# Performance work log

Measured on AMD Instinct MI355X. Metric: run time of the kernel, lower is better.

Reference implementation:

```python
import jax, jax.numpy as jnp
import numpy as np

N_EMBD = 1024
NUM_HEADS = 16
HEAD_SIZE = 64
B, T, T_ENC = 2, 2048, 2048


def setup_inputs() -> dict:
    key = jax.random.key(0)
    k1, k2, k3, k4, k5 = jax.random.split(key, 5)
    scale = 1.0 / np.sqrt(N_EMBD)
    return {
        "x_enc": jax.random.normal(k1, (B, T_ENC, N_EMBD), dtype=jnp.float32),
        "x": jax.random.normal(k2, (B, T, N_EMBD), dtype=jnp.float32),
        "Wk": jax.random.normal(k3, (N_EMBD, NUM_HEADS * HEAD_SIZE), dtype=jnp.float32) * scale,
        "Wq": jax.random.normal(k4, (N_EMBD, NUM_HEADS * HEAD_SIZE), dtype=jnp.float32) * scale,
        "Wv": jax.random.normal(k5, (N_EMBD, NUM_HEADS * HEAD_SIZE), dtype=jnp.float32) * scale,
    }


def reference(x_enc, x, Wk, Wq, Wv):
    b, t, c = x.shape
    _, t_enc, _ = x_enc.shape
    # projections (bias-free linears)
    k = (x_enc @ Wk).reshape(b, t_enc, NUM_HEADS, HEAD_SIZE)  # [B,S,H,D]
    v = (x_enc @ Wv).reshape(b, t_enc, NUM_HEADS, HEAD_SIZE)
    q = (x @ Wq).reshape(b, t, NUM_HEADS, HEAD_SIZE)          # [B,T,H,D]
    # NOTE: original scales by C**-0.5 with C = n_embd (not head_size)
    scale = jnp.asarray(c, x.dtype) ** -0.5
    wei = jnp.einsum("bthd,bshd->bhts", q, k) * scale          # [B,H,T,S]
    wei = jax.nn.softmax(wei, axis=-1)
    out = jnp.einsum("bhts,bshd->bthd", wei, v)                # [B,T,H,D]
    return out
```

## Files before the change

### kernel.cpp

```cpp
#include <hip/hip_runtime.h>
#include <hip/hip_bf16.h>
#include <stdint.h>

#define NE 1024
#define NH 16
#define HD 64
#define BB 2
#define TT 2048
#define MM (BB*TT)

typedef __attribute__((ext_vector_type(8))) short short8;
typedef __attribute__((ext_vector_type(4))) float floatx4;

__device__ __forceinline__ short f2bf(float f) {
    union { float f; uint32_t u; } v; v.f = f;
    uint32_t u = v.u;
    return (short)((u + 0x7fffu + ((u >> 16) & 1u)) >> 16);
}

__device__ __forceinline__ float fast_exp2(float x) {
#if __has_builtin(__builtin_amdgcn_exp2f)
    return __builtin_amdgcn_exp2f(x);
#else
    float r; asm("v_exp_f32 %0, %1" : "=v"(r) : "v"(x)); return r;
#endif
}

__device__ __forceinline__ void gload_lds16(const void* g, void* l) {
    __builtin_amdgcn_global_load_lds((__attribute__((address_space(1))) void*)g,
                                     (__attribute__((address_space(3))) void*)l,
                                     16, 0, 0);
}

__global__ void cvt_bf16(const float* __restrict__ in, short* __restrict__ out, int n8) {
    int i = blockIdx.x * blockDim.x + threadIdx.x;
    if (i >= n8) return;
    const floatx4* p = (const floatx4*)(in + (size_t)i * 8);
    floatx4 a = p[0], b = p[1];
    union { uint32_t u[4]; short8 s; } r;
    asm("v_cvt_pk_bf16_f32 %0, %1, %2" : "=v"(r.u[0]) : "v"(a[0]), "v"(a[1]));
    asm("v_cvt_pk_bf16_f32 %0, %1, %2" : "=v"(r.u[1]) : "v"(a[2]), "v"(a[3]));
    asm("v_cvt_pk_bf16_f32 %0, %1, %2" : "=v"(r.u[2]) : "v"(b[0]), "v"(b[1]));
    asm("v_cvt_pk_bf16_f32 %0, %1, %2" : "=v"(r.u[3]) : "v"(b[2]), "v"(b[3]));
    *(short8*)(out + (size_t)i * 8) = r.s;
}

__global__ void wtrans(const float* __restrict__ Wq, const float* __restrict__ Wk,
                       const float* __restrict__ Wv, short* __restrict__ Wt) {
    __shared__ float t[32][33];
    const float* W = blockIdx.z == 0 ? Wq : (blockIdx.z == 1 ? Wk : Wv);
    short* dst = Wt + (size_t)blockIdx.z * NE * NE;
    int n0 = blockIdx.x * 32, k0 = blockIdx.y * 32;
    int tx = threadIdx.x & 31, ty = threadIdx.x >> 5;
    #pragma unroll
    for (int i = 0; i < 4; i++)
        t[ty * 4 + i][tx] = W[(size_t)(k0 + ty * 4 + i) * NE + n0 + tx];
    __syncthreads();
    #pragma unroll
    for (int i = 0; i < 4; i++)
        dst[(size_t)(n0 + ty * 4 + i) * NE + k0 + tx] = f2bf(t[tx][ty * 4 + i]);
}

__global__ void __launch_bounds__(256) gemm_bt(const short* __restrict__ x_bf,
                                               const short* __restrict__ xenc_bf,
                                               const short* __restrict__ Wt,
                                               short* __restrict__ qkv) {
    __shared__ short sA[3][4096];
    __shared__ short sB[3][4096];
    const int bid = blockIdx.x;
    const int xcd = bid & 7, inner = bid >> 3;
    const int xblk = inner & 7;
    const int yh = (inner >> 3) & 3;
    const int z = inner >> 5;
    const int yblk = xcd + 8 * yh;

    const short* A  = (z == 0) ? x_bf : xenc_bf;
    const short* Bt = Wt + (size_t)z * NE * NE;
    short* C = qkv + (size_t)z * MM * NE;
    const float osc = (z == 0) ? 0.04508422f : 1.0f;

    const int tid = threadIdx.x;
    const int lane = tid & 63, wid = tid >> 6;
    const int l15 = lane & 15, lg = lane >> 4;
    const int wr = wid >> 1, wc = wid & 1;
    const int m0 = yblk * 128, n0 = xblk * 128;

    const short* gA = A  + (size_t)(m0 + (tid >> 2)) * NE + (tid & 3) * 8;
    const short* gB = Bt + (size_t)(n0 + (tid >> 2)) * NE + (tid & 3) * 8;

    floatx4 acc[4][4];
    floatx4 zero = {0.f, 0.f, 0.f, 0.f};
    #pragma unroll
    for (int i = 0; i < 4; i++)
        #pragma unroll
        for (int j = 0; j < 4; j++) acc[i][j] = zero;

#define GSTAGE(bi, kt) do { \
    gload_lds16(gA + (kt),            &sA[bi][wid * 512]); \
    gload_lds16(gA + 64 * NE + (kt),  &sA[bi][wid * 512 + 2048]); \
    gload_lds16(gB + (kt),            &sB[bi][wid * 512]); \
    gload_lds16(gB + 64 * NE + (kt),  &sB[bi][wid * 512 + 2048]); \
} while (0)

#define GCOMP(cur) do { \
    short8 af[4], bfr[4]; \
    _Pragma("unroll") \
    for (int i = 0; i < 4; i++) { \
        af[i]  = *(const short8*)&sA[cur][(wr * 64 + i * 16 + l15) * 32 + lg * 8]; \
        bfr[i] = *(const short8*)&sB[cur][(wc * 64 + i * 16 + l15) * 32 + lg * 8]; \
    } \
    __builtin_amdgcn_s_setprio(1); \
    _Pragma("unroll") \
    for (int i = 0; i < 4; i++) \
        _Pragma("unroll") \
        for (int j = 0; j < 4; j++) \
            acc[i][j] = __builtin_amdgcn_mfma_f32_16x16x32_bf16(af[i], bfr[j], acc[i][j], 0, 0, 0); \
    __builtin_amdgcn_s_setprio(0); \
} while (0)

    GSTAGE(0, 0);
    GSTAGE(1, 32);
    for (int t = 0; t < 31; ++t) {
        asm volatile("s_waitcnt vmcnt(4)" ::: "memory");
        __builtin_amdgcn_sched_barrier(0);
        __builtin_amdgcn_s_barrier();
        __builtin_amdgcn_sched_barrier(0);
        if (t < 30) GSTAGE((t + 2) % 3, (t + 2) * 32);
        GCOMP(t % 3);
    }
    asm volatile("s_waitcnt vmcnt(0)" ::: "memory");
    __builtin_amdgcn_sched_barrier(0);
    __builtin_amdgcn_s_barrier();
    __builtin_amdgcn_sched_barrier(0);
    GCOMP(1);
#undef GSTAGE
#undef GCOMP

    #pragma unroll
    for (int i = 0; i < 4; i++)
        #pragma unroll
        for (int j = 0; j < 4; j++)
            #pragma unroll
            for (int r = 0; r < 4; r++) {
                int row = m0 + wr * 64 + i * 16 + lg * 4 + r;
                int col = n0 + wc * 64 + j * 16 + l15;
                C[(size_t)row * NE + col] = f2bf(acc[i][j][r] * osc);
            }
}

__global__ void vtrans(const short* __restrict__ v, short* __restrict__ vt) {
    __shared__ short t[64][65];
    int s0 = blockIdx.x * 64;
    int bh = blockIdx.y;
    int b = bh >> 4, h = bh & 15;
    int tid = threadIdx.x;
    int c = tid & 63, rr = tid >> 6;
    #pragma unroll
    for (int i = 0; i < 16; i++)
        t[i * 4 + rr][c] = v[(size_t)(b * TT + s0 + i * 4 + rr) * NE + h * HD + c];
    __syncthreads();
    int csw = (c & 35) | (((c >> 4) & 1) << 2) | (((c >> 2) & 3) << 3);
    #pragma unroll
    for (int i = 0; i < 16; i++)
        vt[(size_t)(bh * HD + i * 4 + rr) * TT + s0 + csw] = t[c][i * 4 + rr];
}

__global__ void __launch_bounds__(256, 2) fattn(const short* __restrict__ q,
                                                const short* __restrict__ k,
                                                const short* __restrict__ vt,
                                                float* __restrict__ out) {
    __shared__ short kbuf[3][4096];
    __shared__ short vbuf[3][4096];
    const int tid = threadIdx.x, lane = tid & 63, wid = tid >> 6;
    const int l15 = lane & 15, lg = lane >> 4;
    const int bid = blockIdx.x;
    const int xcd = bid & 7, rest = bid >> 3;
    const int qblk = rest & 15;
    const int bh = xcd + 8 * (rest >> 4);
    const int b = bh >> 4, h = bh & 15;
    const int q0 = qblk * 128 + wid * 32;

    short8 qf[2][2];
    #pragma unroll
    for (int qb = 0; qb < 2; qb++) {
        const short* qp = q + (size_t)(b * TT + q0 + qb * 16 + l15) * NE + h * HD + lg * 8;
        qf[qb][0] = *(const short8*)qp;
        qf[qb][1] = *(const short8*)(qp + 32);
    }
    short8 ones;
    #pragma unroll
    for (int j = 0; j < 8; j++) ones[j] = (short)0x3F80;

    floatx4 acc_o[2][4];
    floatx4 acc_l[2];
    floatx4 zero = {0.f, 0.f, 0.f, 0.f};
    floatx4 minus8 = {-8.f, -8.f, -8.f, -8.f};
    #pragma unroll
    for (int qb = 0; qb < 2; qb++) {
        acc_l[qb] = zero;
        #pragma unroll
        for (int db = 0; db < 4; db++) acc_o[qb][db] = zero;
    }

    const char* kgb = (const char*)(k + (size_t)(b * TT) * NE + h * HD);
    const char* vgb = (const char*)(vt + (size_t)bh * HD * TT);
    const int srow = tid >> 3;
    const int ssw  = ((tid & 7) * 16) ^ ((srow & 7) << 4);
    const char* ksrc = kgb + (size_t)srow * (NE * 2) + ssw;
    const char* vsrc = vgb + (size_t)srow * (TT * 2) + ssw;

    const int swz  = (l15 & 7) << 4;
    const int rd0  = l15 * 128 + ((lg * 16) ^ swz);
    const int rd1  = l15 * 128 + ((64 + lg * 16) ^ swz);

#define STAGE(bi, s0v) do { \
    const char* ks_ = ksrc + (size_t)(s0v) * (NE * 2); \
    gload_lds16(ks_,                 &kbuf[bi][wid * 512]); \
    gload_lds16(ks_ + 32 * (NE * 2), &kbuf[bi][wid * 512 + 2048]); \
    const char* vs_ = vsrc + (size_t)(s0v) * 2; \
    gload_lds16(vs_,                 &vbuf[bi][wid * 512]); \
    gload_lds16(vs_ + 32 * (TT * 2), &vbuf[bi][wid * 512 + 2048]); \
} while (0)

    STAGE(0, 0);
    STAGE(1, 64);
    asm volatile("s_waitcnt vmcnt(4)" ::: "memory");
    __builtin_amdgcn_sched_barrier(0);
    __builtin_amdgcn_s_barrier();
    __builtin_amdgcn_sched_barrier(0);

    short8 kfr[4][2];
    {
        const char* kb = (const char*)kbuf[0];
        #pragma unroll
        for (int cb = 0; cb < 4; cb++) {
            kfr[cb][0] = *(const short8*)(kb + cb * 2048 + rd0);
            kfr[cb][1] = *(const short8*)(kb + cb * 2048 + rd1);
        }
    }

    for (int t = 0; t < 32; ++t) {
        const int cur = t % 3;
        asm volatile("s_waitcnt vmcnt(0)" ::: "memory");
        __builtin_amdgcn_sched_barrier(0);
        __builtin_amdgcn_s_barrier();
        __builtin_amdgcn_sched_barrier(0);
        if (t < 30) STAGE((t + 2) % 3, (t + 2) * 64);

        floatx4 sacc[2][4];
        #pragma unroll
        for (int qb = 0; qb < 2; qb++)
            #pragma unroll
            for (int cb = 0; cb < 4; cb++) sacc[qb][cb] = minus8;
        __builtin_amdgcn_s_setprio(1);
        #pragma unroll
        for (int qb = 0; qb < 2; qb++)
            #pragma unroll
            for (int cb = 0; cb < 4; cb++) {
                sacc[qb][cb] = __builtin_amdgcn_mfma_f32_16x16x32_bf16(kfr[cb][0], qf[qb][0], sacc[qb][cb], 0, 0, 0);
                sacc[qb][cb] = __builtin_amdgcn_mfma_f32_16x16x32_bf16(kfr[cb][1], qf[qb][1], sacc[qb][cb], 0, 0, 0);
            }
        __builtin_amdgcn_s_setprio(0);

        if (t < 31) {
            const char* kb = (const char*)kbuf[(t + 1) % 3];
            #pragma unroll
            for (int cb = 0; cb < 4; cb++) {
                kfr[cb][0] = *(const short8*)(kb + cb * 2048 + rd0);
                kfr[cb][1] = *(const short8*)(kb + cb * 2048 + rd1);
            }
        }

        const char* vb = (const char*)vbuf[cur];
        short8 vf[2][4];
        #pragma unroll
        for (int db = 0; db < 4; db++) {
            vf[0][db] = *(const short8*)(vb + db * 2048 + rd0);
            vf[1][db] = *(const short8*)(vb + db * 2048 + rd1);
        }

        short8 paf[2][2];
        #pragma unroll
        for (int qb = 0; qb < 2; qb++) {
            float pe[16];
            #pragma unroll
            for (int cb = 0; cb < 4; cb++)
                #pragma unroll
                for (int r = 0; r < 4; r++)
                    pe[cb * 4 + r] = fast_exp2(sacc[qb][cb][r]);
            #pragma unroll
            for (int ks = 0; ks < 2; ks++) {
                union { uint32_t u[4]; short8 s; } pk_;
                #pragma unroll
                for (int j2 = 0; j2 < 4; j2++)
                    asm("v_cvt_pk_bf16_f32 %0, %1, %2"
                        : "=v"(pk_.u[j2])
                        : "v"(pe[ks * 8 + 2 * j2]), "v"(pe[ks * 8 + 2 * j2 + 1]));
                paf[qb][ks] = pk_.s;
            }
        }

        __builtin_amdgcn_s_setprio(1);
        #pragma unroll
        for (int qb = 0; qb < 2; qb++)
            #pragma unroll
            for (int ks = 0; ks < 2; ks++) {
                #pragma unroll
                for (int db = 0; db < 4; db++)
                    acc_o[qb][db] = __builtin_amdgcn_mfma_f32_16x16x32_bf16(paf[qb][ks], vf[ks][db], acc_o[qb][db], 0, 0, 0);
                acc_l[qb] = __builtin_amdgcn_mfma_f32_16x16x32_bf16(paf[qb][ks], ones, acc_l[qb], 0, 0, 0);
            }
        __builtin_amdgcn_s_setprio(0);
    }
#undef STAGE

    #pragma unroll
    for (int qb = 0; qb < 2; qb++) {
        #pragma unroll
        for (int r = 0; r < 4; r++) {
            float inv = 1.0f / acc_l[qb][r];
            #pragma unroll
            for (int db = 0; db < 4; db++)
                out[(size_t)(b * TT + q0 + qb * 16 + lg * 4 + r) * NE + h * HD + db * 16 + l15] =
                    acc_o[qb][db][r] * inv;
        }
    }
}

extern "C" void kernel_launch(void* const* d_in, const int* in_sizes, int n_in,
                              void* d_out, int out_size, void* d_ws, size_t ws_size,
                              hipStream_t stream) {
    const float* x_enc = (const float*)d_in[0];
    const float* x     = (const float*)d_in[1];
    const float* Wk    = (const float*)d_in[2];
    const float* Wq    = (const float*)d_in[3];
    const float* Wv    = (const float*)d_in[4];
    float* out = (float*)d_out;

    const size_t SZ = (size_t)MM * NE;
    short* x_bf    = (short*)d_ws;
    short* xenc_bf = x_bf + SZ;
    short* Wt      = xenc_bf + SZ;
    short* qkv     = Wt + 3 * (size_t)NE * NE;
    short* vt      = qkv + 3 * SZ;

    cvt_bf16<<<dim3(2048), dim3(256), 0, stream>>>(x,     x_bf,    (int)(SZ / 8));
    cvt_bf16<<<dim3(2048), dim3(256), 0, stream>>>(x_enc, xenc_bf, (int)(SZ / 8));
    wtrans<<<dim3(32, 32, 3), dim3(256), 0, stream>>>(Wq, Wk, Wv, Wt);
    gemm_bt<<<dim3(768), dim3(256), 0, stream>>>(x_bf, xenc_bf, Wt, qkv);
    vtrans<<<dim3(32, 32), dim3(256), 0, stream>>>(qkv + 2 * SZ, vt);
    fattn<<<dim3(512), dim3(256), 0, stream>>>(qkv, qkv + SZ, vt, out);
}
```

Baseline: 94.80 us.

## Use two-wave 64x128 GEMM tiles, merge bf16 conversion launches, fold query scale into weights

The QKV projection GEMM now runs 128 threads per block. Each of its two waves computes a 64x128 sub-tile, reusing its A fragments across eight B fragments and issuing four staged LDS loads per operand per thread. The two fp32-to-bf16 conversion kernels become one launch, and the softmax scale for the query is applied during the weight transpose instead of in the GEMM epilogue. The aim is to cut LDS traffic per MFMA and launch overhead. The cost is a doubled accumulator register footprint with fewer waves per block, and scaling before the bf16 rounding slightly changes numerics.

```diff
diff --git a/kernel.cpp b/kernel.cpp
--- a/kernel.cpp
+++ b/kernel.cpp
@@ -32,23 +32,27 @@
                                      16, 0, 0);
 }
 
-__global__ void cvt_bf16(const float* __restrict__ in, short* __restrict__ out, int n8) {
+__global__ void cvt_bf16_2(const float* __restrict__ ina, const float* __restrict__ inb,
+                           short* __restrict__ outa, short* __restrict__ outb, int n8half) {
     int i = blockIdx.x * blockDim.x + threadIdx.x;
-    if (i >= n8) return;
-    const floatx4* p = (const floatx4*)(in + (size_t)i * 8);
+    const float* in; short* out; int j;
+    if (i < n8half) { in = ina; out = outa; j = i; }
+    else            { in = inb; out = outb; j = i - n8half; }
+    const floatx4* p = (const floatx4*)(in + (size_t)j * 8);
     floatx4 a = p[0], b = p[1];
     union { uint32_t u[4]; short8 s; } r;
     asm("v_cvt_pk_bf16_f32 %0, %1, %2" : "=v"(r.u[0]) : "v"(a[0]), "v"(a[1]));
     asm("v_cvt_pk_bf16_f32 %0, %1, %2" : "=v"(r.u[1]) : "v"(a[2]), "v"(a[3]));
     asm("v_cvt_pk_bf16_f32 %0, %1, %2" : "=v"(r.u[2]) : "v"(b[0]), "v"(b[1]));
     asm("v_cvt_pk_bf16_f32 %0, %1, %2" : "=v"(r.u[3]) : "v"(b[2]), "v"(b[3]));
-    *(short8*)(out + (size_t)i * 8) = r.s;
+    *(short8*)(out + (size_t)j * 8) = r.s;
 }
 
 __global__ void wtrans(const float* __restrict__ Wq, const float* __restrict__ Wk,
                        const float* __restrict__ Wv, short* __restrict__ Wt) {
     __shared__ float t[32][33];
     const float* W = blockIdx.z == 0 ? Wq : (blockIdx.z == 1 ? Wk : Wv);
+    const float sc = (blockIdx.z == 0) ? 0.04508422f : 1.0f;
     short* dst = Wt + (size_t)blockIdx.z * NE * NE;
     int n0 = blockIdx.x * 32, k0 = blockIdx.y * 32;
     int tx = threadIdx.x & 31, ty = threadIdx.x >> 5;
@@ -58,10 +62,10 @@
     __syncthreads();
     #pragma unroll
     for (int i = 0; i < 4; i++)
-        dst[(size_t)(n0 + ty * 4 + i) * NE + k0 + tx] = f2bf(t[tx][ty * 4 + i]);
-}
-
-__global__ void __launch_bounds__(256) gemm_bt(const short* __restrict__ x_bf,
+        dst[(size_t)(n0 + ty * 4 + i) * NE + k0 + tx] = f2bf(t[tx][ty * 4 + i] * sc);
+}
+
+__global__ void __launch_bounds__(128) gemm_bt(const short* __restrict__ x_bf,
                                                const short* __restrict__ xenc_bf,
                                                const short* __restrict__ Wt,
                                                short* __restrict__ qkv) {
@@ -77,51 +81,55 @@
     const short* A  = (z == 0) ? x_bf : xenc_bf;
     const short* Bt = Wt + (size_t)z * NE * NE;
     short* C = qkv + (size_t)z * MM * NE;
-    const float osc = (z == 0) ? 0.04508422f : 1.0f;
 
     const int tid = threadIdx.x;
     const int lane = tid & 63, wid = tid >> 6;
     const int l15 = lane & 15, lg = lane >> 4;
-    const int wr = wid >> 1, wc = wid & 1;
     const int m0 = yblk * 128, n0 = xblk * 128;
 
     const short* gA = A  + (size_t)(m0 + (tid >> 2)) * NE + (tid & 3) * 8;
     const short* gB = Bt + (size_t)(n0 + (tid >> 2)) * NE + (tid & 3) * 8;
 
-    floatx4 acc[4][4];
+    floatx4 acc[4][8];
     floatx4 zero = {0.f, 0.f, 0.f, 0.f};
     #pragma unroll
     for (int i = 0; i < 4; i++)
         #pragma unroll
-        for (int j = 0; j < 4; j++) acc[i][j] = zero;
+        for (int j = 0; j < 8; j++) acc[i][j] = zero;
 
 #define GSTAGE(bi, kt) do { \
-    gload_lds16(gA + (kt),            &sA[bi][wid * 512]); \
-    gload_lds16(gA + 64 * NE + (kt),  &sA[bi][wid * 512 + 2048]); \
-    gload_lds16(gB + (kt),            &sB[bi][wid * 512]); \
-    gload_lds16(gB + 64 * NE + (kt),  &sB[bi][wid * 512 + 2048]); \
+    _Pragma("unroll") \
+    for (int r_ = 0; r_ < 4; r_++) { \
+        gload_lds16(gA + (size_t)r_ * 32 * NE + (kt), &sA[bi][r_ * 1024 + tid * 8]); \
+        gload_lds16(gB + (size_t)r_ * 32 * NE + (kt), &sB[bi][r_ * 1024 + tid * 8]); \
+    } \
 } while (0)
 
 #define GCOMP(cur) do { \
-    short8 af[4], bfr[4]; \
-    _Pragma("unroll") \
-    for (int i = 0; i < 4; i++) { \
-        af[i]  = *(const short8*)&sA[cur][(wr * 64 + i * 16 + l15) * 32 + lg * 8]; \
-        bfr[i] = *(const short8*)&sB[cur][(wc * 64 + i * 16 + l15) * 32 + lg * 8]; \
-    } \
-    __builtin_amdgcn_s_setprio(1); \
+    short8 af[4]; \
     _Pragma("unroll") \
     for (int i = 0; i < 4; i++) \
+        af[i] = *(const short8*)&sA[cur][(wid * 64 + i * 16 + l15) * 32 + lg * 8]; \
+    _Pragma("unroll") \
+    for (int jh = 0; jh < 2; jh++) { \
+        short8 bfr[4]; \
         _Pragma("unroll") \
         for (int j = 0; j < 4; j++) \
-            acc[i][j] = __builtin_amdgcn_mfma_f32_16x16x32_bf16(af[i], bfr[j], acc[i][j], 0, 0, 0); \
-    __builtin_amdgcn_s_setprio(0); \
+            bfr[j] = *(const short8*)&sB[cur][((jh * 4 + j) * 16 + l15) * 32 + lg * 8]; \
+        __builtin_amdgcn_s_setprio(1); \
+        _Pragma("unroll") \
+        for (int i = 0; i < 4; i++) \
+            _Pragma("unroll") \
+            for (int j = 0; j < 4; j++) \
+                acc[i][jh * 4 + j] = __builtin_amdgcn_mfma_f32_16x16x32_bf16(af[i], bfr[j], acc[i][jh * 4 + j], 0, 0, 0); \
+        __builtin_amdgcn_s_setprio(0); \
+    } \
 } while (0)
 
     GSTAGE(0, 0);
     GSTAGE(1, 32);
     for (int t = 0; t < 31; ++t) {
-        asm volatile("s_waitcnt vmcnt(4)" ::: "memory");
+        asm volatile("s_waitcnt vmcnt(8)" ::: "memory");
         __builtin_amdgcn_sched_barrier(0);
         __builtin_amdgcn_s_barrier();
         __builtin_amdgcn_sched_barrier(0);
@@ -139,12 +147,12 @@
     #pragma unroll
     for (int i = 0; i < 4; i++)
         #pragma unroll
-        for (int j = 0; j < 4; j++)
+        for (int j = 0; j < 8; j++)
             #pragma unroll
             for (int r = 0; r < 4; r++) {
-                int row = m0 + wr * 64 + i * 16 + lg * 4 + r;
-                int col = n0 + wc * 64 + j * 16 + l15;
-                C[(size_t)row * NE + col] = f2bf(acc[i][j][r] * osc);
+                int row = m0 + wid * 64 + i * 16 + lg * 4 + r;
+                int col = n0 + j * 16 + l15;
+                C[(size_t)row * NE + col] = f2bf(acc[i][j][r]);
             }
 }
 
@@ -344,10 +352,9 @@
     short* qkv     = Wt + 3 * (size_t)NE * NE;
     short* vt      = qkv + 3 * SZ;
 
-    cvt_bf16<<<dim3(2048), dim3(256), 0, stream>>>(x,     x_bf,    (int)(SZ / 8));
-    cvt_bf16<<<dim3(2048), dim3(256), 0, stream>>>(x_enc, xenc_bf, (int)(SZ / 8));
+    cvt_bf16_2<<<dim3(4096), dim3(256), 0, stream>>>(x, x_enc, x_bf, xenc_bf, (int)(SZ / 8));
     wtrans<<<dim3(32, 32, 3), dim3(256), 0, stream>>>(Wq, Wk, Wv, Wt);
-    gemm_bt<<<dim3(768), dim3(256), 0, stream>>>(x_bf, xenc_bf, Wt, qkv);
+    gemm_bt<<<dim3(768), dim3(128), 0, stream>>>(x_bf, xenc_bf, Wt, qkv);
     vtrans<<<dim3(32, 32), dim3(256), 0, stream>>>(qkv + 2 * SZ, vt);
     fattn<<<dim3(512), dim3(256), 0, stream>>>(qkv, qkv + SZ, vt, out);
 }
```

Result: no change. 94.83 us (+0.0%).
